# Optimization experiments

Hardware: AMD Instinct MI355X
Metric: run time of the kernel (lower is better)

The kernel has to match this reference:

```python
import jax, jax.numpy as jnp
import numpy as np
from jax import lax

BS, EN, SEQ = 512, 512, 64
D_ENT, D_IN, D_KEY, D_F, H = 256, 1024, 32, 256, 32


def _layer_norm(x, g, b, eps=1e-5):
    m = x.mean(-1, keepdims=True)
    v = ((x - m) ** 2).mean(-1, keepdims=True)
    return (x - m) * lax.rsqrt(v + eps) * g + b


def setup_inputs() -> dict:
    key = jax.random.key(0)
    ks = jax.random.split(key, 24)
    f32 = jnp.float32

    def w(k, shape, fan_in):
        return (jax.random.normal(k, shape, dtype=f32) / np.sqrt(fan_in)).astype(f32)

    inp = {
        'entity_embedding': jax.random.normal(ks[0], (BS, EN, D_ENT), dtype=f32),
        'autoregressive_embedding': jax.random.normal(ks[1], (BS, D_IN), dtype=f32),
        'entity_num': jax.random.randint(ks[2], (BS,), 0, EN),
        'selected_units': jax.random.randint(ks[3], (BS, SEQ), 0, EN),
        'selected_units_num': jax.random.randint(ks[4], (BS,), 0, SEQ),
        # fc_block params (Linear: y = x @ W + b)
        'key_fc_w': w(ks[5], (D_ENT, D_KEY), D_ENT), 'key_fc_b': jnp.zeros((D_KEY,), f32),
        'q1_w': w(ks[6], (D_IN, D_F), D_IN), 'q1_b': jnp.zeros((D_F,), f32),
        'q2_w': w(ks[7], (D_F, D_KEY), D_F), 'q2_b': jnp.zeros((D_KEY,), f32),
        'e1_w': w(ks[8], (D_KEY, D_F), D_KEY), 'e1_b': jnp.zeros((D_F,), f32),
        'e2_w': w(ks[9], (D_F, D_IN), D_F), 'e2_b': jnp.zeros((D_IN,), f32),
        'end_embedding': jax.random.uniform(ks[10], (D_KEY,), dtype=f32,
                                            minval=-1.0 / np.sqrt(D_KEY), maxval=1.0 / np.sqrt(D_KEY)),
        # LayerNorm-LSTM (single layer), gate order: i, f, g, o
        'w_ih': w(ks[11], (D_KEY, 4 * H), D_KEY),
        'w_hh': w(ks[12], (H, 4 * H), H),
        'ln_ig': 1.0 + 0.1 * jax.random.normal(ks[13], (4 * H,), dtype=f32),
        'ln_ib': 0.1 * jax.random.normal(ks[14], (4 * H,), dtype=f32),
        'ln_hg': 1.0 + 0.1 * jax.random.normal(ks[15], (4 * H,), dtype=f32),
        'ln_hb': 0.1 * jax.random.normal(ks[16], (4 * H,), dtype=f32),
        'ln_cg': 1.0 + 0.1 * jax.random.normal(ks[17], (H,), dtype=f32),
        'ln_cb': 0.1 * jax.random.normal(ks[18], (H,), dtype=f32),
    }
    return inp


def _forward(entity_embedding, autoregressive_embedding, entity_num, selected_units,
             selected_units_num, key_fc_w, key_fc_b, q1_w, q1_b, q2_w, q2_b,
             e1_w, e1_b, e2_w, e2_b, end_embedding,
             w_ih, w_hh, ln_ig, ln_ib, ln_hg, ln_hb, ln_cg, ln_cb):
    bs = entity_embedding.shape[0]
    ar = jnp.arange(bs)
    # _get_key_mask: keys for all entities + zero pad slot, end_embedding at slot entity_num
    key = entity_embedding @ key_fc_w + key_fc_b                      # [bs, EN, Dk]
    key = jnp.concatenate([key, jnp.zeros((bs, 1, key.shape[-1]), key.dtype)], axis=1)  # [bs, EN+1, Dk]
    key = key.at[ar, entity_num].set(end_embedding.astype(key.dtype))
    key_embeddings = key                                              # reduce_type == 'selected_units_num'
    base_mask = jnp.arange(key.shape[1])[None, :] < (entity_num + 1)[:, None]  # sequence_mask(entity_num+1)
    mask0 = base_mask.at[ar, entity_num].set(False)                   # end token masked at step 0
    su_prev = jnp.concatenate([selected_units[:, :1], selected_units[:, :-1]], axis=1)

    def step(carry, xs):
        mask, ae, end_flag, one_hot, h, c = carry
        i, su_i, su_p = xs
        # teacher-forced mask evolution
        m1 = jnp.where(i == 1, mask.at[ar, entity_num].set(True), mask)
        m2 = m1.at[ar, su_p].set(False)
        mask = jnp.where(i > 0, m2, mask)
        # query_fc2(query_fc1(ae)) -> LN-LSTM cell
        x = jnp.maximum(ae @ q1_w + q1_b, 0.0) @ q2_w + q2_b
        gates = _layer_norm(x @ w_ih, ln_ig, ln_ib) + _layer_norm(h @ w_hh, ln_hg, ln_hb)
        ig, fg, cg, og = jnp.split(gates, 4, axis=-1)
        c = _layer_norm(jax.nn.sigmoid(fg) * c + jax.nn.sigmoid(ig) * jnp.tanh(cg), ln_cg, ln_cb)
        h = jax.nn.sigmoid(og) * jnp.tanh(c)
        # one-hot scatter of selected unit (skipped once end token seen)
        end_flag = end_flag | (su_i == entity_num)
        one_hot = one_hot.at[ar, su_i].max((~end_flag).astype(one_hot.dtype))
        # mean-pooled embedding of selected units -> embed_fc -> new ae
        emb = jnp.einsum('bn,bnd->bd', one_hot, key_embeddings)
        cnt = one_hot.sum(-1)
        denom = jnp.where((selected_units_num != 0) & (cnt > 0), cnt, 1.0)
        emb = emb / denom[:, None]
        ae = autoregressive_embedding + (jnp.maximum(emb @ e1_w + e1_b, 0.0) @ e2_w + e2_b)
        return (mask, ae, end_flag, one_hot, h, c), (h, mask)

    carry0 = (mask0, autoregressive_embedding,
              jnp.zeros((bs,), bool), jnp.zeros((bs, key.shape[1]), key.dtype),
              jnp.zeros((bs, w_hh.shape[0]), key.dtype), jnp.zeros((bs, w_hh.shape[0]), key.dtype))
    xs = (jnp.arange(selected_units.shape[1]), selected_units.T, su_prev.T)
    _, (queries, masks) = lax.scan(step, carry0, xs)   # [S,bs,Dk], [S,bs,EN+1]
    logits = jnp.einsum('sbd,bnd->sbn', queries, key)
    logits = jnp.where(masks, logits, jnp.asarray(-1e9, logits.dtype))
    return logits.transpose(1, 0, 2)                   # [bs, S, EN+1]


def reference(entity_embedding, autoregressive_embedding, entity_num, selected_units,
              selected_units_num, key_fc_w, key_fc_b, q1_w, q1_b, q2_w, q2_b,
              e1_w, e1_b, e2_w, e2_b, end_embedding,
              w_ih, w_hh, ln_ig, ln_ib, ln_hg, ln_hb, ln_cg, ln_cb):
    return _forward(entity_embedding, autoregressive_embedding, entity_num, selected_units,
                    selected_units_num, key_fc_w, key_fc_b, q1_w, q1_b, q2_w, q2_b,
                    e1_w, e1_b, e2_w, e2_b, end_embedding,
                    w_ih, w_hh, ln_ig, ln_ib, ln_hg, ln_hb, ln_cg, ln_cb)
```

## Files before the change

### kernel.cpp

```cpp
#include <hip/hip_runtime.h>
#include <cstdint>
#include <cstddef>


typedef short bf16x8 __attribute__((ext_vector_type(8)));
typedef float f32x4  __attribute__((ext_vector_type(4)));

__device__ __forceinline__ ushort f2bf(float f) {
    union { float f; unsigned u; } x; x.f = f;
    unsigned r = x.u + 0x7fffu + ((x.u >> 16) & 1u);
    return (ushort)(r >> 16);
}

__device__ __forceinline__ void gld16(const void* g, void* l) {
    __builtin_amdgcn_global_load_lds(
        (const __attribute__((address_space(1))) void*)g,
        (__attribute__((address_space(3))) void*)l,
        16, 0, 0);
}

template<int BM, int BN, int BK, int WR, int WC,
         bool RELU, bool ADDVEC, bool OUT_BF16, bool A_F32, bool KEYMODE>
__global__ __launch_bounds__(WR * WC * 64)
void mfma_gemm(const void* __restrict__ Av, int lda,
               const ushort* __restrict__ BT,
               const float* __restrict__ bias,
               const float* __restrict__ addvec, int ldadd,
               void* __restrict__ outv, int ldo,
               int K, int out_row_offset)
{
    constexpr int NT  = WR * WC * 64;
    constexpr int WM  = BM / WR, WN = BN / WC;
    constexpr int TMt = WM / 16, TNt = WN / 16;
    constexpr int KC  = BK / 8;
    constexpr int CHA = BM * KC, CHB = BN * KC;
    __shared__ __align__(16) ushort As[BM * BK];
    __shared__ __align__(16) ushort Bs[BN * BK];

    const int tid  = threadIdx.x;
    const int lane = tid & 63;
    const int w    = tid >> 6;
    const int wr   = w / WC, wc = w % WC;
    const int row0 = blockIdx.x * BM;
    const int n0   = blockIdx.y * BN;

    f32x4 acc[TMt][TNt];
#pragma unroll
    for (int i = 0; i < TMt; i++)
#pragma unroll
        for (int j = 0; j < TNt; j++)
#pragma unroll
            for (int r = 0; r < 4; r++) acc[i][j][r] = 0.f;

    const ushort* Ab = (const ushort*)Av;
    const float*  Af = (const float*)Av;

    for (int k0 = 0; k0 < K; k0 += BK) {
        if (A_F32) {
#pragma unroll
            for (int id = tid; id < CHA; id += NT) {
                int r = id / KC, kc = id % KC;
                const float* src = Af + (size_t)(row0 + r) * lda + k0 + kc * 8;
                float4 v0 = *(const float4*)(src);
                float4 v1 = *(const float4*)(src + 4);
                bf16x8 p;
                p[0] = (short)f2bf(v0.x); p[1] = (short)f2bf(v0.y);
                p[2] = (short)f2bf(v0.z); p[3] = (short)f2bf(v0.w);
                p[4] = (short)f2bf(v1.x); p[5] = (short)f2bf(v1.y);
                p[6] = (short)f2bf(v1.z); p[7] = (short)f2bf(v1.w);
                *(bf16x8*)(&As[id * 8]) = p;
            }
        } else {
#pragma unroll
            for (int id = tid; id < CHA; id += NT) {
                int r = id / KC, kc = id % KC;
                gld16(Ab + (size_t)(row0 + r) * lda + k0 + kc * 8, &As[id * 8]);
            }
        }
#pragma unroll
        for (int id = tid; id < CHB; id += NT) {
            int r = id / KC, kc = id % KC;
            gld16(BT + (size_t)(n0 + r) * K + k0 + kc * 8, &Bs[id * 8]);
        }
        __syncthreads();

        bf16x8 afr[TMt], bfr[TNt];
        const int krd = (lane >> 4) * 8;
        const int mrd = lane & 15;
#pragma unroll
        for (int tm = 0; tm < TMt; tm++)
            afr[tm] = *(bf16x8*)(&As[(wr * WM + tm * 16 + mrd) * BK + krd]);
#pragma unroll
        for (int tn = 0; tn < TNt; tn++)
            bfr[tn] = *(bf16x8*)(&Bs[(wc * WN + tn * 16 + mrd) * BK + krd]);
#pragma unroll
        for (int tm = 0; tm < TMt; tm++)
#pragma unroll
            for (int tn = 0; tn < TNt; tn++)
                acc[tm][tn] = __builtin_amdgcn_mfma_f32_16x16x32_bf16(
                    afr[tm], bfr[tn], acc[tm][tn], 0, 0, 0);
        __syncthreads();
    }

    float*  outf = (float*)outv;
    ushort* outh = (ushort*)outv;
    const int cn = lane & 15;
    const int rb = (lane >> 4) * 4;
#pragma unroll
    for (int tm = 0; tm < TMt; tm++) {
#pragma unroll
        for (int r = 0; r < 4; r++) {
            int grow = row0 + wr * WM + tm * 16 + rb + r;
            int b_   = grow & 511;
#pragma unroll
            for (int tn = 0; tn < TNt; tn++) {
                int gcol = n0 + wc * WN + tn * 16 + cn;
                float v = acc[tm][tn][r] + bias[gcol];
                if (RELU)   v = fmaxf(v, 0.f);
                if (ADDVEC) v += addvec[(size_t)b_ * ldadd + gcol];
                size_t oidx;
                if (KEYMODE) oidx = ((size_t)(grow >> 9) * 513 + b_) * 32 + gcol;
                else         oidx = (size_t)(grow + out_row_offset) * ldo + gcol;
                if (OUT_BF16) outh[oidx] = f2bf(v);
                else          outf[oidx] = v;
            }
        }
    }
}

__global__ __launch_bounds__(256) void wt_cvt(const float* __restrict__ W,
                                              ushort* __restrict__ WT, int K, int N)
{
    __shared__ float t[32][33];
    int kt = blockIdx.x * 32, nt = blockIdx.y * 32;
    int x = threadIdx.x & 31, y = threadIdx.x >> 5;
    for (int i = y; i < 32; i += 8) t[i][x] = W[(size_t)(kt + i) * N + nt + x];
    __syncthreads();
    for (int i = y; i < 32; i += 8) WT[(size_t)(nt + i) * K + kt + x] = f2bf(t[x][i]);
}

__global__ void key_fixup(const int* __restrict__ en, const float* __restrict__ eemb,
                          float* __restrict__ key)
{
    int b = blockIdx.x;
    int t = threadIdx.x;
    key[((size_t)b * 513 + 512) * 32 + t] = 0.f;
    key[((size_t)b * 513 + en[b]) * 32 + t] = eemb[t];
}

__global__ __launch_bounds__(64) void prep_kernel(
    const int* __restrict__ en_g, const int* __restrict__ su_g,
    const int* __restrict__ sun_g, const float* __restrict__ key,
    int* __restrict__ fs_g, ushort* __restrict__ EMB)
{
    int b = blockIdx.x;
    int tid = threadIdx.x;
    __shared__ int fs_l[513];
    __shared__ int su_l[64];
    for (int i = tid; i < 513; i += 64) fs_l[i] = 64;
    su_l[tid] = su_g[b * 64 + tid];
    __syncthreads();
    atomicMin(&fs_l[su_l[tid]], tid);
    int en = en_g[b];
    unsigned long long ball = __ballot(su_l[tid] == en);
    int T = ball ? (__ffsll(ball) - 1) : 64;
    __syncthreads();
    for (int i = tid; i < 513; i += 64) fs_g[(size_t)b * 513 + i] = fs_l[i];

    int sun = sun_g[b];
    float a = 0.f;
    int cnt = 0;
    for (int i = 0; i < 64; i++) {
        int su_i = su_l[i];
        bool nw = (i < T) && (fs_l[su_i] == i);
        if (nw) {
            cnt++;
            if (tid < 32) a += key[((size_t)b * 513 + su_i) * 32 + tid];
        }
        float denom = (sun != 0 && cnt > 0) ? (float)cnt : 1.0f;
        if (tid < 32) EMB[((size_t)i * 512 + b) * 32 + tid] = f2bf(a / denom);
    }
}

__global__ void ae_init(const float* __restrict__ ar, ushort* __restrict__ AEb)
{
    int i = (blockIdx.x * blockDim.x + threadIdx.x) * 4;
    float4 v = *(const float4*)(ar + i);
    ushort4 o;
    o.x = f2bf(v.x); o.y = f2bf(v.y); o.z = f2bf(v.z); o.w = f2bf(v.w);
    *(ushort4*)(AEb + i) = o;
}

__device__ inline float wave_sum64(float v)
{
#pragma unroll
    for (int m = 1; m <= 32; m <<= 1) v += __shfl_xor(v, m, 64);
    return v;
}
__device__ inline float sigm(float x) { return 1.0f / (1.0f + expf(-x)); }

__global__ __launch_bounds__(128) void lstm_kernel(
    const float* __restrict__ X, const float* __restrict__ wih_g,
    const float* __restrict__ whh_g,
    const float* __restrict__ lnig, const float* __restrict__ lnib,
    const float* __restrict__ lnhg, const float* __restrict__ lnhb,
    const float* __restrict__ lncg, const float* __restrict__ lncb,
    float* __restrict__ Q)
{
    int b = blockIdx.x;
    int tid = threadIdx.x;
    int lane = tid & 63, wv = tid >> 6;
    __shared__ float wih[32 * 128], whh[32 * 128];
    for (int i = tid; i < 4096; i += 128) { wih[i] = wih_g[i]; whh[i] = whh_g[i]; }
    __shared__ float xv[32], hv[32], cv[32], gl[128], red[8];
    if (tid < 32) { hv[tid] = 0.f; cv[tid] = 0.f; }
    float gi = lnig[tid], bi = lnib[tid], gh = lnhg[tid], bh = lnhb[tid];
    float gc = 0.f, bc = 0.f;
    if (tid < 32) { gc = lncg[tid]; bc = lncb[tid]; }
    __syncthreads();

    for (int s = 0; s < 64; s++) {
        if (tid < 32) xv[tid] = X[((size_t)s * 512 + b) * 32 + tid];
        __syncthreads();
        float ax = 0.f, ah = 0.f;
#pragma unroll
        for (int k = 0; k < 32; k++) {
            ax += xv[k] * wih[k * 128 + tid];
            ah += hv[k] * whh[k * 128 + tid];
        }
        float s0 = wave_sum64(ax), s1 = wave_sum64(ax * ax);
        float s2 = wave_sum64(ah), s3 = wave_sum64(ah * ah);
        if (lane == 0) { red[wv*4+0]=s0; red[wv*4+1]=s1; red[wv*4+2]=s2; red[wv*4+3]=s3; }
        __syncthreads();
        float mx = (red[0] + red[4]) * (1.f/128.f);
        float vx = (red[1] + red[5]) * (1.f/128.f) - mx * mx;
        float mh = (red[2] + red[6]) * (1.f/128.f);
        float vh = (red[3] + red[7]) * (1.f/128.f) - mh * mh;
        float gate = (ax - mx) * rsqrtf(vx + 1e-5f) * gi + bi
                   + (ah - mh) * rsqrtf(vh + 1e-5f) * gh + bh;
        gl[tid] = gate;
        __syncthreads();
        if (tid < 32) {
            float igv = gl[tid], fgv = gl[32 + tid], cgv = gl[64 + tid], ogv = gl[96 + tid];
            float cc = sigm(fgv) * cv[tid] + sigm(igv) * tanhf(cgv);
            float u0 = cc, u1 = cc * cc;
#pragma unroll
            for (int m = 1; m <= 16; m <<= 1) {
                u0 += __shfl_xor(u0, m, 32);
                u1 += __shfl_xor(u1, m, 32);
            }
            float mc = u0 * (1.f/32.f);
            float vc = u1 * (1.f/32.f) - mc * mc;
            float cn = (cc - mc) * rsqrtf(vc + 1e-5f) * gc + bc;
            float hn = sigm(ogv) * tanhf(cn);
            cv[tid] = cn; hv[tid] = hn;
            Q[((size_t)b * 64 + s) * 32 + tid] = hn;
        }
        __syncthreads();
    }
}

__global__ __launch_bounds__(128) void logits_kernel(
    const float* __restrict__ key, const float* __restrict__ Q,
    const int* __restrict__ fs_g, const int* __restrict__ en_g,
    float* __restrict__ out)
{
    int b = blockIdx.x;
    int n0 = blockIdx.y * 128;
    int tid = threadIdx.x;
    __shared__ float Qs[64 * 32];
    __shared__ float Ks[128 * 33];
    for (int i = tid * 4; i < 2048; i += 512)
        *(float4*)(&Qs[i]) = *(const float4*)(Q + (size_t)b * 2048 + i);
    for (int i = tid; i < 4096; i += 128) {
        int r = i >> 5, d = i & 31;
        int n = n0 + r;
        Ks[r * 33 + d] = (n < 513) ? key[((size_t)b * 513 + n) * 32 + d] : 0.f;
    }
    __syncthreads();
    int n = n0 + tid;
    if (n < 513) {
        int en = en_g[b];
        int f = fs_g[(size_t)b * 513 + n];
        float kreg[32];
#pragma unroll
        for (int d = 0; d < 32; d++) kreg[d] = Ks[tid * 33 + d];
        for (int s = 0; s < 64; s++) {
            float a = 0.f;
#pragma unroll
            for (int d = 0; d < 32; d++) a += Qs[s * 32 + d] * kreg[d];
            bool m = (s == 0) ? (n < en) : ((n <= en) && (f >= s));
            out[((size_t)b * 64 + s) * 513 + n] = m ? a : -1e9f;
        }
    }
}

extern "C" void kernel_launch(void* const* d_in, const int* in_sizes, int n_in,
                              void* d_out, int out_size, void* d_ws, size_t ws_size,
                              hipStream_t stream)
{
    const float* ee   = (const float*)d_in[0];
    const float* ar   = (const float*)d_in[1];
    const int*   en   = (const int*)d_in[2];
    const int*   su   = (const int*)d_in[3];
    const int*   sun  = (const int*)d_in[4];
    const float* kw   = (const float*)d_in[5];
    const float* kb   = (const float*)d_in[6];
    const float* q1w  = (const float*)d_in[7];
    const float* q1b  = (const float*)d_in[8];
    const float* q2w  = (const float*)d_in[9];
    const float* q2b  = (const float*)d_in[10];
    const float* e1w  = (const float*)d_in[11];
    const float* e1b  = (const float*)d_in[12];
    const float* e2w  = (const float*)d_in[13];
    const float* e2b  = (const float*)d_in[14];
    const float* eemb = (const float*)d_in[15];
    const float* wih  = (const float*)d_in[16];
    const float* whh  = (const float*)d_in[17];
    const float* lnig = (const float*)d_in[18];
    const float* lnib = (const float*)d_in[19];
    const float* lnhg = (const float*)d_in[20];
    const float* lnhb = (const float*)d_in[21];
    const float* lncg = (const float*)d_in[22];
    const float* lncb = (const float*)d_in[23];
    float* outp = (float*)d_out;

    char* p = (char*)d_ws;
    float*  key  = (float*)p;  p += (size_t)512 * 513 * 32 * 4;
    ushort* AEb  = (ushort*)p; p += (size_t)32768 * 1024 * 2;
    ushort* Z1b  = (ushort*)p; p += (size_t)32768 * 256 * 2;
    ushort* EMBb = (ushort*)p; p += (size_t)32768 * 32 * 2;
    float*  X    = (float*)p;  p += (size_t)32768 * 32 * 4;
    float*  Q    = (float*)p;  p += (size_t)32768 * 32 * 4;
    int*    fs   = (int*)p;    p += (size_t)512 * 513 * 4;
    ushort* kwt  = (ushort*)p; p += (size_t)32 * 256 * 2;
    ushort* e1wt = (ushort*)p; p += (size_t)256 * 32 * 2;
    ushort* e2wt = (ushort*)p; p += (size_t)1024 * 256 * 2;
    ushort* q1wt = (ushort*)p; p += (size_t)256 * 1024 * 2;
    ushort* q2wt = (ushort*)p; p += (size_t)32 * 256 * 2;

    wt_cvt<<<dim3(8, 1),  256, 0, stream>>>(kw,  kwt,  256, 32);
    wt_cvt<<<dim3(1, 8),  256, 0, stream>>>(e1w, e1wt, 32, 256);
    wt_cvt<<<dim3(8, 32), 256, 0, stream>>>(e2w, e2wt, 256, 1024);
    wt_cvt<<<dim3(32, 8), 256, 0, stream>>>(q1w, q1wt, 1024, 256);
    wt_cvt<<<dim3(8, 1),  256, 0, stream>>>(q2w, q2wt, 256, 32);

    mfma_gemm<128, 32, 32, 4, 1, false, false, false, true, true>
        <<<dim3(2048, 1), 256, 0, stream>>>(ee, 256, kwt, kb, nullptr, 0, key, 32, 256, 0);
    key_fixup<<<512, 32, 0, stream>>>(en, eemb, key);
    prep_kernel<<<512, 64, 0, stream>>>(en, su, sun, key, fs, EMBb);

    mfma_gemm<128, 128, 32, 2, 2, true, false, true, false, false>
        <<<dim3(252, 2), 256, 0, stream>>>(EMBb, 32, e1wt, e1b, nullptr, 0, Z1b, 256, 32, 0);
    ae_init<<<512, 256, 0, stream>>>(ar, AEb);
    mfma_gemm<128, 128, 32, 2, 2, false, true, true, false, false>
        <<<dim3(252, 8), 256, 0, stream>>>(Z1b, 256, e2wt, e2b, ar, 1024, AEb, 1024, 256, 512);
    mfma_gemm<128, 128, 32, 2, 2, true, false, true, false, false>
        <<<dim3(256, 2), 256, 0, stream>>>(AEb, 1024, q1wt, q1b, nullptr, 0, Z1b, 256, 1024, 0);
    mfma_gemm<128, 32, 32, 4, 1, false, false, false, false, false>
        <<<dim3(256, 1), 256, 0, stream>>>(Z1b, 256, q2wt, q2b, nullptr, 0, X, 32, 256, 0);

    lstm_kernel<<<512, 128, 0, stream>>>(X, wih, whh, lnig, lnib, lnhg, lnhb, lncg, lncb, Q);

    logits_kernel<<<dim3(512, 5), 128, 0, stream>>>(key, Q, fs, en, outp);
}
```

Baseline: 767.2 us.

## Run one LSTM wave per batch with register weights; merge small prep kernels

The LSTM kernel now assigns one 64-lane wave per batch element. Both weight matrices live in registers, and the hidden state is exchanged by lane shuffles, so the per-step block barriers and shared-memory round trips are gone. Weight transposes and the autoregressive-embedding conversion are merged into one launch. The key fixup is folded into the prep kernel, which also stages the selected key rows in LDS. The cost is much higher register use per LSTM thread, which may lower occupancy, and half as many LSTM blocks.

Measured after the change: 701.8 us. 1.09x faster.

```diff
diff --git a/kernel.cpp b/kernel.cpp
--- a/kernel.cpp
+++ b/kernel.cpp
@@ -128,75 +128,86 @@
     }
 }
 
-__global__ __launch_bounds__(256) void wt_cvt(const float* __restrict__ W,
-                                              ushort* __restrict__ WT, int K, int N)
-{
+__global__ __launch_bounds__(256) void misc_prep(
+    const float* __restrict__ kw,  const float* __restrict__ e1w,
+    const float* __restrict__ e2w, const float* __restrict__ q1w,
+    const float* __restrict__ q2w,
+    ushort* __restrict__ kwt,  ushort* __restrict__ e1wt,
+    ushort* __restrict__ e2wt, ushort* __restrict__ q1wt,
+    ushort* __restrict__ q2wt,
+    const float* __restrict__ ar, ushort* __restrict__ AEb)
+{
+    int bx = blockIdx.x;
+    if (bx < 512) {
+        int i = (bx * 256 + threadIdx.x) * 4;
+        float4 v = *(const float4*)(ar + i);
+        ushort4 o;
+        o.x = f2bf(v.x); o.y = f2bf(v.y); o.z = f2bf(v.z); o.w = f2bf(v.w);
+        *(ushort4*)(AEb + i) = o;
+        return;
+    }
+    bx -= 512;
+    const float* W; ushort* WT; int K, N, t0;
+    if      (bx < 8)   { W = kw;  WT = kwt;  K = 256;  N = 32;   t0 = bx; }
+    else if (bx < 16)  { W = e1w; WT = e1wt; K = 32;   N = 256;  t0 = bx - 8; }
+    else if (bx < 272) { W = e2w; WT = e2wt; K = 256;  N = 1024; t0 = bx - 16; }
+    else if (bx < 528) { W = q1w; WT = q1wt; K = 1024; N = 256;  t0 = bx - 272; }
+    else               { W = q2w; WT = q2wt; K = 256;  N = 32;   t0 = bx - 528; }
+    int nn = N >> 5;
+    int kt = (t0 / nn) * 32, nt = (t0 % nn) * 32;
     __shared__ float t[32][33];
-    int kt = blockIdx.x * 32, nt = blockIdx.y * 32;
     int x = threadIdx.x & 31, y = threadIdx.x >> 5;
     for (int i = y; i < 32; i += 8) t[i][x] = W[(size_t)(kt + i) * N + nt + x];
     __syncthreads();
     for (int i = y; i < 32; i += 8) WT[(size_t)(nt + i) * K + kt + x] = f2bf(t[x][i]);
 }
 
-__global__ void key_fixup(const int* __restrict__ en, const float* __restrict__ eemb,
-                          float* __restrict__ key)
-{
-    int b = blockIdx.x;
-    int t = threadIdx.x;
-    key[((size_t)b * 513 + 512) * 32 + t] = 0.f;
-    key[((size_t)b * 513 + en[b]) * 32 + t] = eemb[t];
-}
-
 __global__ __launch_bounds__(64) void prep_kernel(
     const int* __restrict__ en_g, const int* __restrict__ su_g,
-    const int* __restrict__ sun_g, const float* __restrict__ key,
+    const int* __restrict__ sun_g, float* __restrict__ key,
+    const float* __restrict__ eemb,
     int* __restrict__ fs_g, ushort* __restrict__ EMB)
 {
     int b = blockIdx.x;
     int tid = threadIdx.x;
     __shared__ int fs_l[513];
     __shared__ int su_l[64];
+    __shared__ float krows[64 * 32];
     for (int i = tid; i < 513; i += 64) fs_l[i] = 64;
     su_l[tid] = su_g[b * 64 + tid];
+    int en = en_g[b];
+    if (tid < 32) key[((size_t)b * 513 + 512) * 32 + tid] = 0.f;
+    else          key[((size_t)b * 513 + en) * 32 + (tid - 32)] = eemb[tid - 32];
     __syncthreads();
     atomicMin(&fs_l[su_l[tid]], tid);
-    int en = en_g[b];
     unsigned long long ball = __ballot(su_l[tid] == en);
     int T = ball ? (__ffsll(ball) - 1) : 64;
     __syncthreads();
+    {
+        int d = tid & 31;
+#pragma unroll 4
+        for (int i = 0; i < 32; i++) {
+            int r = 2 * i + (tid >> 5);
+            krows[r * 32 + d] = key[((size_t)b * 513 + su_l[r]) * 32 + d];
+        }
+    }
     for (int i = tid; i < 513; i += 64) fs_g[(size_t)b * 513 + i] = fs_l[i];
+    __syncthreads();
 
     int sun = sun_g[b];
     float a = 0.f;
     int cnt = 0;
     for (int i = 0; i < 64; i++) {
-        int su_i = su_l[i];
-        bool nw = (i < T) && (fs_l[su_i] == i);
+        bool nw = (i < T) && (fs_l[su_l[i]] == i);
         if (nw) {
             cnt++;
-            if (tid < 32) a += key[((size_t)b * 513 + su_i) * 32 + tid];
+            if (tid < 32) a += krows[i * 32 + tid];
         }
         float denom = (sun != 0 && cnt > 0) ? (float)cnt : 1.0f;
         if (tid < 32) EMB[((size_t)i * 512 + b) * 32 + tid] = f2bf(a / denom);
     }
 }
 
-__global__ void ae_init(const float* __restrict__ ar, ushort* __restrict__ AEb)
-{
-    int i = (blockIdx.x * blockDim.x + threadIdx.x) * 4;
-    float4 v = *(const float4*)(ar + i);
-    ushort4 o;
-    o.x = f2bf(v.x); o.y = f2bf(v.y); o.z = f2bf(v.z); o.w = f2bf(v.w);
-    *(ushort4*)(AEb + i) = o;
-}
-
-__device__ inline float wave_sum64(float v)
-{
-#pragma unroll
-    for (int m = 1; m <= 32; m <<= 1) v += __shfl_xor(v, m, 64);
-    return v;
-}
 __device__ inline float sigm(float x) { return 1.0f / (1.0f + expf(-x)); }
 
 __global__ __launch_bounds__(128) void lstm_kernel(
@@ -207,56 +218,70 @@
     const float* __restrict__ lncg, const float* __restrict__ lncb,
     float* __restrict__ Q)
 {
-    int b = blockIdx.x;
-    int tid = threadIdx.x;
-    int lane = tid & 63, wv = tid >> 6;
-    __shared__ float wih[32 * 128], whh[32 * 128];
-    for (int i = tid; i < 4096; i += 128) { wih[i] = wih_g[i]; whh[i] = whh_g[i]; }
-    __shared__ float xv[32], hv[32], cv[32], gl[128], red[8];
-    if (tid < 32) { hv[tid] = 0.f; cv[tid] = 0.f; }
-    float gi = lnig[tid], bi = lnib[tid], gh = lnhg[tid], bh = lnhb[tid];
-    float gc = 0.f, bc = 0.f;
-    if (tid < 32) { gc = lncg[tid]; bc = lncb[tid]; }
-    __syncthreads();
-
+    const int wv = threadIdx.x >> 6;
+    const int lane = threadIdx.x & 63;
+    const int b = blockIdx.x * 2 + wv;
+    __shared__ float xs[2][64 * 32];
+
+    {
+        int d = lane & 31;
+#pragma unroll 8
+        for (int i = 0; i < 32; i++) {
+            int s = 2 * i + (lane >> 5);
+            xs[wv][s * 32 + d] = X[((size_t)s * 512 + b) * 32 + d];
+        }
+    }
+    float w0[32], w1[32], u0[32], u1[32];
+#pragma unroll
+    for (int k = 0; k < 32; k++) {
+        w0[k] = wih_g[k * 128 + lane];
+        w1[k] = wih_g[k * 128 + lane + 64];
+        u0[k] = whh_g[k * 128 + lane];
+        u1[k] = whh_g[k * 128 + lane + 64];
+    }
+    const float gi0 = lnig[lane], gi1 = lnig[lane + 64];
+    const float bi0 = lnib[lane], bi1 = lnib[lane + 64];
+    const float gh0 = lnhg[lane], gh1 = lnhg[lane + 64];
+    const float bh0 = lnhb[lane], bh1 = lnhb[lane + 64];
+    const int j = lane & 31;
+    const float gc = lncg[j], bc = lncb[j];
+    float h = 0.f, c = 0.f;
+    __syncthreads();
+
+    const float* xrow = &xs[wv][0];
     for (int s = 0; s < 64; s++) {
-        if (tid < 32) xv[tid] = X[((size_t)s * 512 + b) * 32 + tid];
-        __syncthreads();
-        float ax = 0.f, ah = 0.f;
+        float ax0 = 0.f, ax1 = 0.f, ah0 = 0.f, ah1 = 0.f;
 #pragma unroll
         for (int k = 0; k < 32; k++) {
-            ax += xv[k] * wih[k * 128 + tid];
-            ah += hv[k] * whh[k * 128 + tid];
-        }
-        float s0 = wave_sum64(ax), s1 = wave_sum64(ax * ax);
-        float s2 = wave_sum64(ah), s3 = wave_sum64(ah * ah);
-        if (lane == 0) { red[wv*4+0]=s0; red[wv*4+1]=s1; red[wv*4+2]=s2; red[wv*4+3]=s3; }
-        __syncthreads();
-        float mx = (red[0] + red[4]) * (1.f/128.f);
-        float vx = (red[1] + red[5]) * (1.f/128.f) - mx * mx;
-        float mh = (red[2] + red[6]) * (1.f/128.f);
-        float vh = (red[3] + red[7]) * (1.f/128.f) - mh * mh;
-        float gate = (ax - mx) * rsqrtf(vx + 1e-5f) * gi + bi
-                   + (ah - mh) * rsqrtf(vh + 1e-5f) * gh + bh;
-        gl[tid] = gate;
-        __syncthreads();
-        if (tid < 32) {
-            float igv = gl[tid], fgv = gl[32 + tid], cgv = gl[64 + tid], ogv = gl[96 + tid];
-            float cc = sigm(fgv) * cv[tid] + sigm(igv) * tanhf(cgv);
-            float u0 = cc, u1 = cc * cc;
-#pragma unroll
-            for (int m = 1; m <= 16; m <<= 1) {
-                u0 += __shfl_xor(u0, m, 32);
-                u1 += __shfl_xor(u1, m, 32);
-            }
-            float mc = u0 * (1.f/32.f);
-            float vc = u1 * (1.f/32.f) - mc * mc;
-            float cn = (cc - mc) * rsqrtf(vc + 1e-5f) * gc + bc;
-            float hn = sigm(ogv) * tanhf(cn);
-            cv[tid] = cn; hv[tid] = hn;
-            Q[((size_t)b * 64 + s) * 32 + tid] = hn;
-        }
-        __syncthreads();
+            float xk = xrow[s * 32 + k];
+            float hk = __shfl(h, k);
+            ax0 += xk * w0[k]; ax1 += xk * w1[k];
+            ah0 += hk * u0[k]; ah1 += hk * u1[k];
+        }
+        float r0 = ax0 + ax1, r1 = ax0 * ax0 + ax1 * ax1;
+        float r2 = ah0 + ah1, r3 = ah0 * ah0 + ah1 * ah1;
+#pragma unroll
+        for (int m = 1; m <= 32; m <<= 1) {
+            r0 += __shfl_xor(r0, m); r1 += __shfl_xor(r1, m);
+            r2 += __shfl_xor(r2, m); r3 += __shfl_xor(r3, m);
+        }
+        float mx = r0 * (1.f / 128.f), vx = r1 * (1.f / 128.f) - mx * mx;
+        float mh = r2 * (1.f / 128.f), vh = r3 * (1.f / 128.f) - mh * mh;
+        float sx = rsqrtf(vx + 1e-5f), sh = rsqrtf(vh + 1e-5f);
+        float g0 = (ax0 - mx) * sx * gi0 + bi0 + (ah0 - mh) * sh * gh0 + bh0;
+        float g1 = (ax1 - mx) * sx * gi1 + bi1 + (ah1 - mh) * sh * gh1 + bh1;
+        float igv = __shfl(g0, j),      fgv = __shfl(g0, j + 32);
+        float cgv = __shfl(g1, j),      ogv = __shfl(g1, j + 32);
+        float cc = sigm(fgv) * c + sigm(igv) * tanhf(cgv);
+        float s0 = cc, s1 = cc * cc;
+#pragma unroll
+        for (int m = 1; m <= 32; m <<= 1) {
+            s0 += __shfl_xor(s0, m); s1 += __shfl_xor(s1, m);
+        }
+        float mc = s0 * (1.f / 64.f), vc = s1 * (1.f / 64.f) - mc * mc;
+        c = (cc - mc) * rsqrtf(vc + 1e-5f) * gc + bc;
+        h = sigm(ogv) * tanhf(c);
+        if (lane < 32) Q[((size_t)b * 64 + s) * 32 + lane] = h;
     }
 }
 
@@ -339,20 +364,15 @@
     ushort* q1wt = (ushort*)p; p += (size_t)256 * 1024 * 2;
     ushort* q2wt = (ushort*)p; p += (size_t)32 * 256 * 2;
 
-    wt_cvt<<<dim3(8, 1),  256, 0, stream>>>(kw,  kwt,  256, 32);
-    wt_cvt<<<dim3(1, 8),  256, 0, stream>>>(e1w, e1wt, 32, 256);
-    wt_cvt<<<dim3(8, 32), 256, 0, stream>>>(e2w, e2wt, 256, 1024);
-    wt_cvt<<<dim3(32, 8), 256, 0, stream>>>(q1w, q1wt, 1024, 256);
-    wt_cvt<<<dim3(8, 1),  256, 0, stream>>>(q2w, q2wt, 256, 32);
+    misc_prep<<<1048, 256, 0, stream>>>(kw, e1w, e2w, q1w, q2w,
+                                        kwt, e1wt, e2wt, q1wt, q2wt, ar, AEb);
 
     mfma_gemm<128, 32, 32, 4, 1, false, false, false, true, true>
         <<<dim3(2048, 1), 256, 0, stream>>>(ee, 256, kwt, kb, nullptr, 0, key, 32, 256, 0);
-    key_fixup<<<512, 32, 0, stream>>>(en, eemb, key);
-    prep_kernel<<<512, 64, 0, stream>>>(en, su, sun, key, fs, EMBb);
+    prep_kernel<<<512, 64, 0, stream>>>(en, su, sun, key, eemb, fs, EMBb);
 
     mfma_gemm<128, 128, 32, 2, 2, true, false, true, false, false>
         <<<dim3(252, 2), 256, 0, stream>>>(EMBb, 32, e1wt, e1b, nullptr, 0, Z1b, 256, 32, 0);
-    ae_init<<<512, 256, 0, stream>>>(ar, AEb);
     mfma_gemm<128, 128, 32, 2, 2, false, true, true, false, false>
         <<<dim3(252, 8), 256, 0, stream>>>(Z1b, 256, e2wt, e2b, ar, 1024, AEb, 1024, 256, 512);
     mfma_gemm<128, 128, 32, 2, 2, true, false, true, false, false>
@@ -360,7 +380,7 @@
     mfma_gemm<128, 32, 32, 4, 1, false, false, false, false, false>
         <<<dim3(256, 1), 256, 0, stream>>>(Z1b, 256, q2wt, q2b, nullptr, 0, X, 32, 256, 0);
 
-    lstm_kernel<<<512, 128, 0, stream>>>(X, wih, whh, lnig, lnib, lnhg, lnhb, lncg, lncb, Q);
+    lstm_kernel<<<256, 128, 0, stream>>>(X, wih, whh, lnig, lnib, lnhg, lnhb, lncg, lncb, Q);
 
     logits_kernel<<<dim3(512, 5), 128, 0, stream>>>(key, Q, fs, en, outp);
 }
```
